# Performance work log

Hardware: AMD Instinct MI355X
Metric: run time of the kernel (lower is better)

Reference implementation:

```python
import jax, jax.numpy as jnp
import numpy as np

H = 16      # num_attention_heads
HKV = 4     # num_key_value_heads
HIDDEN = 1024
HEAD_DIM = HIDDEN // H  # 64
ROPE_BASE = 10000.0


def _rope(x):
    # Rotate-half RoPE applied over the FULL projected last dim, matching the
    # module which applies self._rope before splitting into heads.
    B, S, D = x.shape
    half = D // 2
    inv_freq = 1.0 / (ROPE_BASE ** (jnp.arange(half, dtype=jnp.float32) / half))
    ang = jnp.arange(S, dtype=jnp.float32)[:, None] * inv_freq[None, :]  # [S, half]
    cos, sin = jnp.cos(ang), jnp.sin(ang)
    x1, x2 = x[..., :half], x[..., half:]
    return jnp.concatenate([x1 * cos - x2 * sin, x2 * cos + x1 * sin], axis=-1)


def _rmsnorm(x):
    # F.rms_norm with no weight: x / sqrt(mean(x^2) + eps)
    eps = jnp.finfo(x.dtype).eps
    return x * jax.lax.rsqrt(jnp.mean(x * x, axis=-1, keepdims=True) + eps)


def setup_inputs() -> dict:
    key = jax.random.key(0)
    ks = jax.random.split(key, 10)
    B, S = 2, 2048
    kv_dim = HKV * HEAD_DIM
    sc = 0.02
    return {
        "hidden_state": jax.random.normal(ks[0], (B, S, HIDDEN), dtype=jnp.float32),
        "attention_mask": jnp.zeros((B, S, S), dtype=jnp.float32),
        "Wq": jax.random.normal(ks[1], (HIDDEN, HIDDEN), dtype=jnp.float32) * sc,
        "bq": jnp.zeros((HIDDEN,), dtype=jnp.float32),
        "Wk": jax.random.normal(ks[2], (HIDDEN, kv_dim), dtype=jnp.float32) * sc,
        "bk": jnp.zeros((kv_dim,), dtype=jnp.float32),
        "Wv": jax.random.normal(ks[3], (HIDDEN, kv_dim), dtype=jnp.float32) * sc,
        "bv": jnp.zeros((kv_dim,), dtype=jnp.float32),
        "Wo": jax.random.normal(ks[4], (HIDDEN, HIDDEN), dtype=jnp.float32) * sc,
        "bo": jnp.zeros((HIDDEN,), dtype=jnp.float32),
    }


def reference(hidden_state, attention_mask, Wq, bq, Wk, bk, Wv, bv, Wo, bo):
    B, S, _ = hidden_state.shape
    G = H // HKV  # query heads per kv head
    d = HEAD_DIM

    q = hidden_state @ Wq + bq            # [B,S,H*d]
    k = hidden_state @ Wk + bk            # [B,S,Hkv*d]
    v = hidden_state @ Wv + bv            # [B,S,Hkv*d]

    q = _rope(q)
    k = _rope(k)

    # split heads; repeat_interleave of KV over groups == grouping Q heads as [Hkv, G]
    q = q.reshape(B, S, H, d).transpose(0, 2, 1, 3).reshape(B, HKV, G, S, d)
    k = k.reshape(B, S, HKV, d).transpose(0, 2, 1, 3)   # [B,Hkv,S,d]
    v = v.reshape(B, S, HKV, d).transpose(0, 2, 1, 3)   # [B,Hkv,S,d]

    q = _rmsnorm(q)
    k = _rmsnorm(k)

    scale = d ** 0.5
    scores = jnp.einsum('bkgqd,bksd->bkgqs', q, k) / scale  # [B,Hkv,G,S,S]
    scores = scores + attention_mask[:, None, None, :, :]
    attn = jax.nn.softmax(scores, axis=-1)
    out = jnp.einsum('bkgqs,bksd->bkgqd', attn, v)          # [B,Hkv,G,S,d]

    out = out.reshape(B, H, S, d).transpose(0, 2, 1, 3).reshape(B, S, H * d)
    return out @ Wo + bo
```

## Files before the change

### kernel.cpp

```cpp
#include <hip/hip_runtime.h>
#include <cmath>

#define SEQ 2048
#define BATCH 2
#define HID 1024
#define NH 16
#define NKV 4
#define DH 64
#define KVDIM 256
#define K32C 32

typedef __attribute__((ext_vector_type(8))) short bf16x8;
typedef __attribute__((ext_vector_type(4))) float f32x4;

static __device__ __forceinline__ unsigned short f2bf(float x) {
  union { float f; unsigned u; } v; v.f = x;
  unsigned r = v.u + 0x7fffu + ((v.u >> 16) & 1u);
  return (unsigned short)(r >> 16);
}
static __device__ __forceinline__ float bf2f(unsigned short h) {
  union { unsigned u; float f; } v; v.u = ((unsigned)h) << 16;
  return v.f;
}
static __device__ __forceinline__ void gl_lds16(const unsigned short* g, unsigned short* l) {
  __builtin_amdgcn_global_load_lds(
      (const __attribute__((address_space(1))) unsigned int*)g,
      (__attribute__((address_space(3))) unsigned int*)l, 16, 0, 0);
}

template<bool HILO>
__global__ __launch_bounds__(256) void pack_a_kernel(
    const float* __restrict__ A, unsigned short* __restrict__ hi,
    unsigned short* __restrict__ lo) {
  int gid = blockIdx.x * 256 + threadIdx.x;
  int lane = gid & 63;
  int k32 = (gid >> 6) & 31;
  int m16 = gid >> 11;
  int quad = lane >> 4, l16 = lane & 15;
  const float* src = A + (size_t)(m16 * 16 + l16) * 1024 + k32 * 32 + quad * 8;
  float4 a0 = *(const float4*)src;
  float4 a1 = *(const float4*)(src + 4);
  float v[8] = {a0.x, a0.y, a0.z, a0.w, a1.x, a1.y, a1.z, a1.w};
  unsigned short h[8], l[8];
#pragma unroll
  for (int j = 0; j < 8; ++j) {
    h[j] = f2bf(v[j]);
    if (HILO) l[j] = f2bf(v[j] - bf2f(h[j]));
  }
  *(bf16x8*)(hi + (size_t)gid * 8) = *(bf16x8*)h;
  if (HILO) *(bf16x8*)(lo + (size_t)gid * 8) = *(bf16x8*)l;
}

__global__ __launch_bounds__(256) void pack_a_norm_kernel(
    const float* __restrict__ A, const float* __restrict__ lpart,
    unsigned short* __restrict__ hi, unsigned short* __restrict__ lo) {
  int gid = blockIdx.x * 256 + threadIdx.x;
  int lane = gid & 63;
  int k32 = (gid >> 6) & 31;
  int m16 = gid >> 11;
  int quad = lane >> 4, l16 = lane & 15;
  int m = m16 * 16 + l16;
  int b = m >> 11, s = m & 2047;
  int k0 = k32 * 32 + quad * 8;
  int h = k0 >> 6;
  float inv = 1.0f / lpart[(size_t)(b * NH + h) * SEQ + s];
  const float* src = A + (size_t)m * 1024 + k0;
  float4 a0 = *(const float4*)src;
  float4 a1 = *(const float4*)(src + 4);
  float v[8] = {a0.x, a0.y, a0.z, a0.w, a1.x, a1.y, a1.z, a1.w};
  unsigned short hh[8], ll[8];
#pragma unroll
  for (int j = 0; j < 8; ++j) {
    float x = v[j] * inv;
    hh[j] = f2bf(x);
    ll[j] = f2bf(x - bf2f(hh[j]));
  }
  *(bf16x8*)(hi + (size_t)gid * 8) = *(bf16x8*)hh;
  *(bf16x8*)(lo + (size_t)gid * 8) = *(bf16x8*)ll;
}

template<bool HILO>
__global__ __launch_bounds__(256) void pack_b_kernel(
    const float* __restrict__ W, unsigned short* __restrict__ hi,
    unsigned short* __restrict__ lo, int Nsrc) {
  int gid = blockIdx.x * 256 + threadIdx.x;
  int lane = gid & 63;
  int k32 = (gid >> 6) & 31;
  int n16 = gid >> 11;
  int quad = lane >> 4, l16 = lane & 15;
  int n = n16 * 16 + l16, k = k32 * 32 + quad * 8;
  unsigned short h[8], l[8];
#pragma unroll
  for (int j = 0; j < 8; ++j) {
    float v = W[(size_t)(k + j) * Nsrc + n];
    h[j] = f2bf(v);
    if (HILO) l[j] = f2bf(v - bf2f(h[j]));
  }
  *(bf16x8*)(hi + (size_t)gid * 8) = *(bf16x8*)h;
  if (HILO) *(bf16x8*)(lo + (size_t)gid * 8) = *(bf16x8*)l;
}

__global__ __launch_bounds__(256) void bias_cat_kernel(
    const float* __restrict__ bq, const float* __restrict__ bk,
    const float* __restrict__ bv, float* __restrict__ dst) {
  int n = blockIdx.x * 256 + threadIdx.x;
  if (n < 1536)
    dst[n] = (n < 1024) ? bq[n] : (n < 1280 ? bk[n - 1024] : bv[n - 1280]);
}

template<int CHAINS, bool OUTBF16>
__global__ __launch_bounds__(256) void gemm_pk_kernel(
    const unsigned short* __restrict__ Ah, const unsigned short* __restrict__ Al,
    const unsigned short* __restrict__ Bh, const unsigned short* __restrict__ Bl,
    const float* __restrict__ bias, void* __restrict__ Cout, int N) {
  constexpr int NCH = (CHAINS == 3) ? 2 : 1;
  __shared__ unsigned short Asm[NCH][4 * 512];
  __shared__ unsigned short Bsm[NCH][8 * 512];
  const int tid = threadIdx.x;
  const int wave = tid >> 6, lane = tid & 63;
  const int wr = wave >> 1, wc = wave & 1;
  const int quad = lane >> 4, l16 = lane & 15;
  const size_t abase = ((size_t)(blockIdx.y * 4 + wave) * K32C) * 64 + lane;
  const size_t bbase0 = ((size_t)(blockIdx.x * 8 + wave) * K32C) * 64 + lane;
  const size_t bbase1 = ((size_t)(blockIdx.x * 8 + wave + 4) * K32C) * 64 + lane;
  f32x4 acc[2][4] = {};
  for (int k32 = 0; k32 < K32C; ++k32) {
    __syncthreads();
    gl_lds16(Ah + (abase + (size_t)k32 * 64) * 8, &Asm[0][wave * 512]);
    gl_lds16(Bh + (bbase0 + (size_t)k32 * 64) * 8, &Bsm[0][wave * 512]);
    gl_lds16(Bh + (bbase1 + (size_t)k32 * 64) * 8, &Bsm[0][(wave + 4) * 512]);
    if (CHAINS == 3) {
      gl_lds16(Al + (abase + (size_t)k32 * 64) * 8, &Asm[1][wave * 512]);
      gl_lds16(Bl + (bbase0 + (size_t)k32 * 64) * 8, &Bsm[1][wave * 512]);
      gl_lds16(Bl + (bbase1 + (size_t)k32 * 64) * 8, &Bsm[1][(wave + 4) * 512]);
    }
    __syncthreads();
    bf16x8 af[2][NCH], bfr[4][NCH];
#pragma unroll
    for (int mt = 0; mt < 2; ++mt)
#pragma unroll
      for (int ch = 0; ch < NCH; ++ch)
        af[mt][ch] = *(const bf16x8*)&Asm[ch][((wr * 2 + mt) * 64 + lane) * 8];
#pragma unroll
    for (int nt = 0; nt < 4; ++nt)
#pragma unroll
      for (int ch = 0; ch < NCH; ++ch)
        bfr[nt][ch] = *(const bf16x8*)&Bsm[ch][((wc * 4 + nt) * 64 + lane) * 8];
#pragma unroll
    for (int mt = 0; mt < 2; ++mt)
#pragma unroll
      for (int nt = 0; nt < 4; ++nt) {
        acc[mt][nt] = __builtin_amdgcn_mfma_f32_16x16x32_bf16(af[mt][0], bfr[nt][0], acc[mt][nt], 0, 0, 0);
        if (CHAINS == 3) {
          acc[mt][nt] = __builtin_amdgcn_mfma_f32_16x16x32_bf16(af[mt][1], bfr[nt][0], acc[mt][nt], 0, 0, 0);
          acc[mt][nt] = __builtin_amdgcn_mfma_f32_16x16x32_bf16(af[mt][0], bfr[nt][1], acc[mt][nt], 0, 0, 0);
        }
      }
  }
  const int n0 = blockIdx.x * 128 + wc * 64;
  const int m0 = blockIdx.y * 64 + wr * 32;
#pragma unroll
  for (int mt = 0; mt < 2; ++mt)
#pragma unroll
    for (int nt = 0; nt < 4; ++nt)
#pragma unroll
      for (int r = 0; r < 4; ++r) {
        int gm = m0 + mt * 16 + quad * 4 + r;
        int n = n0 + nt * 16 + l16;
        float v = acc[mt][nt][r] + bias[n];
        if (OUTBF16)
          ((unsigned short*)Cout)[(size_t)gm * N + n] = f2bf(v);
        else
          ((float*)Cout)[(size_t)gm * N + n] = v;
      }
}

__global__ __launch_bounds__(1024) void rope_norm_q_kernel(
    const unsigned short* __restrict__ qkv, unsigned short* __restrict__ Qh,
    unsigned short* __restrict__ Ql) {
  const int s = blockIdx.x, b = blockIdx.y;
  const int t = threadIdx.x;
  const unsigned short* row = qkv + ((size_t)b * SEQ + s) * 1536;
  const int j = t & 511;
  float invf = exp2f((float)j * (-13.287712379549449f / 512.0f));
  float ang = (float)s * invf;
  float c = cosf(ang), sn = sinf(ang);
  float x1 = bf2f(row[j]), x2 = bf2f(row[j + 512]);
  float val = (t < 512) ? (x1 * c - x2 * sn) : (x2 * c + x1 * sn);
  float ss = val * val;
#pragma unroll
  for (int off = 1; off < 64; off <<= 1) ss += __shfl_xor(ss, off);
  float rn = rsqrtf(ss * (1.0f / 64.0f) + 1.1920929e-07f);
  float v = val * rn;
  unsigned short hi = f2bf(v);
  unsigned short lo = f2bf(v - bf2f(hi));
  int h = t >> 6, d = t & 63;
  size_t o = (size_t)(b * NH + h) * 131072 +
             ((((size_t)(s >> 4) * 2 + (d >> 5)) * 64) + ((d >> 3) & 3) * 16 + (s & 15)) * 8 + (d & 7);
  Qh[o] = hi;
  Ql[o] = lo;
}

__global__ __launch_bounds__(256) void rope_norm_kv_kernel(
    const unsigned short* __restrict__ qkv, unsigned short* __restrict__ Kpk,
    unsigned short* __restrict__ Vpk) {
  const int s = blockIdx.x, b = blockIdx.y;
  const int t = threadIdx.x;
  const unsigned short* row = qkv + ((size_t)b * SEQ + s) * 1536;
  const int j = t & 127;
  float invf = exp2f((float)j * (-13.287712379549449f / 128.0f));
  float ang = (float)s * invf;
  float c = cosf(ang), sn = sinf(ang);
  float x1 = bf2f(row[1024 + j]), x2 = bf2f(row[1024 + 128 + j]);
  float val = (t < 128) ? (x1 * c - x2 * sn) : (x2 * c + x1 * sn);
  float ss = val * val;
#pragma unroll
  for (int off = 1; off < 64; off <<= 1) ss += __shfl_xor(ss, off);
  float rn = rsqrtf(ss * (1.0f / 64.0f) + 1.1920929e-07f);
  float kv = val * rn;
  int h = t >> 6, d = t & 63;
  size_t ko = (size_t)(b * NKV + h) * 131072 +
              ((((size_t)(s >> 4) * 2 + (d >> 5)) * 64) + ((d >> 3) & 3) * 16 + (s & 15)) * 8 + (d & 7);
  Kpk[ko] = f2bf(kv);
  size_t vo = (size_t)(b * NKV + h) * 131072 +
              ((((size_t)(d >> 4) * 64 + (s >> 5)) * 64) + ((s >> 3) & 3) * 16 + (d & 15)) * 8 + (s & 7);
  Vpk[vo] = row[1280 + t];
}

__global__ __launch_bounds__(256, 4) void attn_mfma2_kernel(
    const unsigned short* __restrict__ Qh, const unsigned short* __restrict__ Ql,
    const unsigned short* __restrict__ Kpk, const unsigned short* __restrict__ Vpk,
    const float* __restrict__ mask, float* __restrict__ attn_po,
    float* __restrict__ l_part) {
  __shared__ unsigned short Kb[4 * 512];
  __shared__ unsigned short Vb[4 * 512];
  __shared__ float Msk[32][36];
  __shared__ unsigned short Ps[4][32 * 72];

  const int b = blockIdx.z;
  const int kvh = blockIdx.y >> 1, jh = blockIdx.y & 1;
  const int q0 = blockIdx.x * 32;
  const int tid = threadIdx.x, wave = tid >> 6, lane = tid & 63;
  const int quad = lane >> 4, l16 = lane & 15;
  const int h = kvh * 4 + wave;

  bf16x8 qh[2][2], ql[2][2];
  {
    const unsigned short* Qb_h = Qh + (size_t)(b * NH + h) * 131072;
    const unsigned short* Qb_l = Ql + (size_t)(b * NH + h) * 131072;
#pragma unroll
    for (int mt = 0; mt < 2; ++mt)
#pragma unroll
      for (int kf = 0; kf < 2; ++kf) {
        size_t o = ((((size_t)(q0 >> 4) + mt) * 2 + kf) * 64 + lane) * 8;
        qh[mt][kf] = *(const bf16x8*)(Qb_h + o);
        ql[mt][kf] = *(const bf16x8*)(Qb_l + o);
      }
  }

  const unsigned short* Kbase = Kpk + (size_t)(b * NKV + kvh) * 131072;
  const unsigned short* Vbase = Vpk + (size_t)(b * NKV + kvh) * 131072;

  bf16x8 ones;
#pragma unroll
  for (int i = 0; i < 8; ++i) ones[i] = (short)0x3F80;

  f32x4 O[2][4] = {};
  f32x4 lAcc[2] = {};

  const int jbase = jh * (SEQ / 2);
  for (int jc = 0; jc < 32; ++jc) {
    const int j0 = jbase + jc * 32;
    __syncthreads();
    {
      gl_lds16(Kbase + ((((size_t)(j0 >> 4) + (wave >> 1)) * 2 + (wave & 1)) * 64 + lane) * 8,
               &Kb[wave * 512]);
      gl_lds16(Vbase + (((size_t)wave * 64 + (j0 >> 5)) * 64 + lane) * 8,
               &Vb[wave * 512]);
      int mr = tid >> 3, c4 = tid & 7;
      float4 m4 = *(const float4*)(mask + ((size_t)b * SEQ + q0 + mr) * SEQ + j0 + c4 * 4);
      Msk[mr][c4 * 4 + 0] = m4.x - 8.0f;
      Msk[mr][c4 * 4 + 1] = m4.y - 8.0f;
      Msk[mr][c4 * 4 + 2] = m4.z - 8.0f;
      Msk[mr][c4 * 4 + 3] = m4.w - 8.0f;
    }
    __syncthreads();

    bf16x8 kbf[2][2], vbf[4];
#pragma unroll
    for (int nt = 0; nt < 2; ++nt)
#pragma unroll
      for (int kf = 0; kf < 2; ++kf)
        kbf[nt][kf] = *(const bf16x8*)&Kb[((nt * 2 + kf) * 64 + lane) * 8];
#pragma unroll
    for (int d16 = 0; d16 < 4; ++d16)
      vbf[d16] = *(const bf16x8*)&Vb[(d16 * 64 + lane) * 8];

#pragma unroll
    for (int mt = 0; mt < 2; ++mt)
#pragma unroll
      for (int nt = 0; nt < 2; ++nt) {
        f32x4 C = {};
        C = __builtin_amdgcn_mfma_f32_16x16x32_bf16(qh[mt][0], kbf[nt][0], C, 0, 0, 0);
        C = __builtin_amdgcn_mfma_f32_16x16x32_bf16(qh[mt][1], kbf[nt][1], C, 0, 0, 0);
        C = __builtin_amdgcn_mfma_f32_16x16x32_bf16(ql[mt][0], kbf[nt][0], C, 0, 0, 0);
        C = __builtin_amdgcn_mfma_f32_16x16x32_bf16(ql[mt][1], kbf[nt][1], C, 0, 0, 0);
#pragma unroll
        for (int r = 0; r < 4; ++r) {
          int row = mt * 16 + quad * 4 + r;
          float p = __expf(fmaf(C[r], 0.125f, Msk[row][nt * 16 + l16]));
          union { float f; unsigned u; } pu; pu.f = p;
          Ps[wave][row * 72 + nt * 16 + l16] = (unsigned short)((pu.u + 0x8000u) >> 16);
        }
      }

    bf16x8 pa[2];
#pragma unroll
    for (int mt = 0; mt < 2; ++mt)
      pa[mt] = *(const bf16x8*)&Ps[wave][(mt * 16 + l16) * 72 + quad * 8];
#pragma unroll
    for (int mt = 0; mt < 2; ++mt) {
      lAcc[mt] = __builtin_amdgcn_mfma_f32_16x16x32_bf16(pa[mt], ones, lAcc[mt], 0, 0, 0);
#pragma unroll
      for (int nt = 0; nt < 4; ++nt)
        O[mt][nt] = __builtin_amdgcn_mfma_f32_16x16x32_bf16(pa[mt], vbf[nt], O[mt][nt], 0, 0, 0);
    }
  }

#pragma unroll
  for (int mt = 0; mt < 2; ++mt)
#pragma unroll
    for (int r = 0; r < 4; ++r) {
      int s = q0 + mt * 16 + quad * 4 + r;
#pragma unroll
      for (int nt = 0; nt < 4; ++nt)
        atomicAdd(attn_po + ((size_t)b * SEQ + s) * HID + h * DH + nt * 16 + l16,
                  O[mt][nt][r]);
      if (l16 == 0)
        atomicAdd(l_part + (size_t)(b * NH + h) * SEQ + s, lAcc[mt][r]);
    }
}

extern "C" void kernel_launch(void* const* d_in, const int* in_sizes, int n_in,
                              void* d_out, int out_size, void* d_ws, size_t ws_size,
                              hipStream_t stream) {
  const float* hs   = (const float*)d_in[0];
  const float* mask = (const float*)d_in[1];
  const float* Wq   = (const float*)d_in[2];
  const float* bq   = (const float*)d_in[3];
  const float* Wk   = (const float*)d_in[4];
  const float* bk   = (const float*)d_in[5];
  const float* Wv   = (const float*)d_in[6];
  const float* bv   = (const float*)d_in[7];
  const float* Wo   = (const float*)d_in[8];
  const float* bo   = (const float*)d_in[9];
  float* out = (float*)d_out;
  char* ws = (char*)d_ws;
  const size_t MiB = 1048576;

  unsigned short* hs_pk   = (unsigned short*)(ws);
  unsigned short* qkvproj = (unsigned short*)(ws + 8 * MiB);
  float*          attn_po = (float*)(ws);
  float*          l_part  = (float*)(ws + 16 * MiB);
  unsigned short* Wqkv_hi = (unsigned short*)(ws + 20 * MiB);
  unsigned short* Wo_hi   = (unsigned short*)(ws + 20 * MiB);
  unsigned short* Wo_lo   = (unsigned short*)(ws + 22 * MiB);
  unsigned short* Qpk_h   = (unsigned short*)(ws + 24 * MiB);
  unsigned short* Qpk_l   = (unsigned short*)(ws + 32 * MiB);
  unsigned short* ao_hi   = (unsigned short*)(ws + 24 * MiB);
  unsigned short* ao_lo   = (unsigned short*)(ws + 32 * MiB);
  unsigned short* Kpk     = (unsigned short*)(ws + 40 * MiB);
  unsigned short* Vpk     = (unsigned short*)(ws + 42 * MiB);
  float*          bias_c  = (float*)(ws + 44 * MiB);

  pack_a_kernel<false><<<2048, 256, 0, stream>>>(hs, hs_pk, nullptr);
  pack_b_kernel<false><<<512, 256, 0, stream>>>(Wq, Wqkv_hi, nullptr, 1024);
  pack_b_kernel<false><<<128, 256, 0, stream>>>(Wk, Wqkv_hi + (size_t)64 * 2048 * 8, nullptr, 256);
  pack_b_kernel<false><<<128, 256, 0, stream>>>(Wv, Wqkv_hi + (size_t)80 * 2048 * 8, nullptr, 256);
  bias_cat_kernel<<<6, 256, 0, stream>>>(bq, bk, bv, bias_c);

  gemm_pk_kernel<1, true><<<dim3(12, 64), 256, 0, stream>>>(
      hs_pk, nullptr, Wqkv_hi, nullptr, bias_c, qkvproj, 1536);

  pack_b_kernel<true><<<512, 256, 0, stream>>>(Wo, Wo_hi, Wo_lo, 1024);

  rope_norm_q_kernel<<<dim3(SEQ, BATCH), dim3(1024), 0, stream>>>(qkvproj, Qpk_h, Qpk_l);
  rope_norm_kv_kernel<<<dim3(SEQ, BATCH), dim3(256), 0, stream>>>(qkvproj, Kpk, Vpk);

  hipMemsetAsync(ws, 0, 16 * MiB + 262144, stream);
  attn_mfma2_kernel<<<dim3(SEQ / 32, NKV * 2, BATCH), 256, 0, stream>>>(
      Qpk_h, Qpk_l, Kpk, Vpk, mask, attn_po, l_part);

  pack_a_norm_kernel<<<2048, 256, 0, stream>>>(attn_po, l_part, ao_hi, ao_lo);
  gemm_pk_kernel<3, false><<<dim3(8, 64), 256, 0, stream>>>(
      ao_hi, ao_lo, Wo_hi, Wo_lo, bo, out, 1024);
}
```

Baseline: 283.4 us.

## Double-buffer LDS tiles in GEMM and attention, load mask into registers

Both the packed GEMM and the attention kernel now keep two LDS buffers. The next K-chunk (or K/V tile) is issued right after the barrier, while MFMA work runs on the current buffer. This removes the second barrier per iteration and is meant to hide global-to-LDS load latency. The attention kernel also drops the shared mask tile: each lane reads its mask values from global memory straight into registers, saving LDS traffic and a barrier at the cost of less coalesced loads and twice the LDS footprint for K/V, which may affect occupancy.

```diff
diff --git a/kernel.cpp b/kernel.cpp
--- a/kernel.cpp
+++ b/kernel.cpp
@@ -114,8 +114,8 @@
     const unsigned short* __restrict__ Bh, const unsigned short* __restrict__ Bl,
     const float* __restrict__ bias, void* __restrict__ Cout, int N) {
   constexpr int NCH = (CHAINS == 3) ? 2 : 1;
-  __shared__ unsigned short Asm[NCH][4 * 512];
-  __shared__ unsigned short Bsm[NCH][8 * 512];
+  __shared__ unsigned short Asm[2][NCH][4 * 512];
+  __shared__ unsigned short Bsm[2][NCH][8 * 512];
   const int tid = threadIdx.x;
   const int wave = tid >> 6, lane = tid & 63;
   const int wr = wave >> 1, wc = wave & 1;
@@ -124,28 +124,35 @@
   const size_t bbase0 = ((size_t)(blockIdx.x * 8 + wave) * K32C) * 64 + lane;
   const size_t bbase1 = ((size_t)(blockIdx.x * 8 + wave + 4) * K32C) * 64 + lane;
   f32x4 acc[2][4] = {};
+
+  auto stage = [&](int buf, int k32) {
+    gl_lds16(Ah + (abase + (size_t)k32 * 64) * 8, &Asm[buf][0][wave * 512]);
+    gl_lds16(Bh + (bbase0 + (size_t)k32 * 64) * 8, &Bsm[buf][0][wave * 512]);
+    gl_lds16(Bh + (bbase1 + (size_t)k32 * 64) * 8, &Bsm[buf][0][(wave + 4) * 512]);
+    if (CHAINS == 3) {
+      gl_lds16(Al + (abase + (size_t)k32 * 64) * 8, &Asm[buf][1][wave * 512]);
+      gl_lds16(Bl + (bbase0 + (size_t)k32 * 64) * 8, &Bsm[buf][1][wave * 512]);
+      gl_lds16(Bl + (bbase1 + (size_t)k32 * 64) * 8, &Bsm[buf][1][(wave + 4) * 512]);
+    }
+  };
+
+  stage(0, 0);
   for (int k32 = 0; k32 < K32C; ++k32) {
+    const int cur = k32 & 1;
     __syncthreads();
-    gl_lds16(Ah + (abase + (size_t)k32 * 64) * 8, &Asm[0][wave * 512]);
-    gl_lds16(Bh + (bbase0 + (size_t)k32 * 64) * 8, &Bsm[0][wave * 512]);
-    gl_lds16(Bh + (bbase1 + (size_t)k32 * 64) * 8, &Bsm[0][(wave + 4) * 512]);
-    if (CHAINS == 3) {
-      gl_lds16(Al + (abase + (size_t)k32 * 64) * 8, &Asm[1][wave * 512]);
-      gl_lds16(Bl + (bbase0 + (size_t)k32 * 64) * 8, &Bsm[1][wave * 512]);
-      gl_lds16(Bl + (bbase1 + (size_t)k32 * 64) * 8, &Bsm[1][(wave + 4) * 512]);
-    }
-    __syncthreads();
+    if (k32 < K32C - 1) stage(cur ^ 1, k32 + 1);
+
     bf16x8 af[2][NCH], bfr[4][NCH];
 #pragma unroll
     for (int mt = 0; mt < 2; ++mt)
 #pragma unroll
       for (int ch = 0; ch < NCH; ++ch)
-        af[mt][ch] = *(const bf16x8*)&Asm[ch][((wr * 2 + mt) * 64 + lane) * 8];
+        af[mt][ch] = *(const bf16x8*)&Asm[cur][ch][((wr * 2 + mt) * 64 + lane) * 8];
 #pragma unroll
     for (int nt = 0; nt < 4; ++nt)
 #pragma unroll
       for (int ch = 0; ch < NCH; ++ch)
-        bfr[nt][ch] = *(const bf16x8*)&Bsm[ch][((wc * 4 + nt) * 64 + lane) * 8];
+        bfr[nt][ch] = *(const bf16x8*)&Bsm[cur][ch][((wc * 4 + nt) * 64 + lane) * 8];
 #pragma unroll
     for (int mt = 0; mt < 2; ++mt)
 #pragma unroll
@@ -227,14 +234,13 @@
   Vpk[vo] = row[1280 + t];
 }
 
-__global__ __launch_bounds__(256, 4) void attn_mfma2_kernel(
+__global__ __launch_bounds__(256, 4) void attn_mfma3_kernel(
     const unsigned short* __restrict__ Qh, const unsigned short* __restrict__ Ql,
     const unsigned short* __restrict__ Kpk, const unsigned short* __restrict__ Vpk,
     const float* __restrict__ mask, float* __restrict__ attn_po,
     float* __restrict__ l_part) {
-  __shared__ unsigned short Kb[4 * 512];
-  __shared__ unsigned short Vb[4 * 512];
-  __shared__ float Msk[32][36];
+  __shared__ unsigned short Kb[2][4 * 512];
+  __shared__ unsigned short Vb[2][4 * 512];
   __shared__ unsigned short Ps[4][32 * 72];
 
   const int b = blockIdx.z;
@@ -260,6 +266,10 @@
 
   const unsigned short* Kbase = Kpk + (size_t)(b * NKV + kvh) * 131072;
   const unsigned short* Vbase = Vpk + (size_t)(b * NKV + kvh) * 131072;
+  const int jbase = jh * (SEQ / 2);
+
+  const float* mbase = mask + ((size_t)b * SEQ + q0) * SEQ + jbase;
+  const int mlane = (quad * 4) * SEQ + l16;
 
   bf16x8 ones;
 #pragma unroll
@@ -268,33 +278,40 @@
   f32x4 O[2][4] = {};
   f32x4 lAcc[2] = {};
 
-  const int jbase = jh * (SEQ / 2);
+  auto stage = [&](int buf, int jc) {
+    const int j0 = jbase + jc * 32;
+    gl_lds16(Kbase + ((((size_t)(j0 >> 4) + (wave >> 1)) * 2 + (wave & 1)) * 64 + lane) * 8,
+             &Kb[buf][wave * 512]);
+    gl_lds16(Vbase + (((size_t)wave * 64 + (j0 >> 5)) * 64 + lane) * 8,
+             &Vb[buf][wave * 512]);
+  };
+
+  stage(0, 0);
   for (int jc = 0; jc < 32; ++jc) {
-    const int j0 = jbase + jc * 32;
+    const int cur = jc & 1;
     __syncthreads();
-    {
-      gl_lds16(Kbase + ((((size_t)(j0 >> 4) + (wave >> 1)) * 2 + (wave & 1)) * 64 + lane) * 8,
-               &Kb[wave * 512]);
-      gl_lds16(Vbase + (((size_t)wave * 64 + (j0 >> 5)) * 64 + lane) * 8,
-               &Vb[wave * 512]);
-      int mr = tid >> 3, c4 = tid & 7;
-      float4 m4 = *(const float4*)(mask + ((size_t)b * SEQ + q0 + mr) * SEQ + j0 + c4 * 4);
-      Msk[mr][c4 * 4 + 0] = m4.x - 8.0f;
-      Msk[mr][c4 * 4 + 1] = m4.y - 8.0f;
-      Msk[mr][c4 * 4 + 2] = m4.z - 8.0f;
-      Msk[mr][c4 * 4 + 3] = m4.w - 8.0f;
-    }
-    __syncthreads();
+
+    float msub[2][2][4];
+#pragma unroll
+    for (int mt = 0; mt < 2; ++mt)
+#pragma unroll
+      for (int nt = 0; nt < 2; ++nt)
+#pragma unroll
+        for (int r = 0; r < 4; ++r)
+          msub[mt][nt][r] =
+              mbase[(size_t)(mt * 16 + r) * SEQ + mlane + jc * 32 + nt * 16] - 8.0f;
+
+    if (jc < 31) stage(cur ^ 1, jc + 1);
 
     bf16x8 kbf[2][2], vbf[4];
 #pragma unroll
     for (int nt = 0; nt < 2; ++nt)
 #pragma unroll
       for (int kf = 0; kf < 2; ++kf)
-        kbf[nt][kf] = *(const bf16x8*)&Kb[((nt * 2 + kf) * 64 + lane) * 8];
+        kbf[nt][kf] = *(const bf16x8*)&Kb[cur][((nt * 2 + kf) * 64 + lane) * 8];
 #pragma unroll
     for (int d16 = 0; d16 < 4; ++d16)
-      vbf[d16] = *(const bf16x8*)&Vb[(d16 * 64 + lane) * 8];
+      vbf[d16] = *(const bf16x8*)&Vb[cur][(d16 * 64 + lane) * 8];
 
 #pragma unroll
     for (int mt = 0; mt < 2; ++mt)
@@ -308,7 +325,7 @@
 #pragma unroll
         for (int r = 0; r < 4; ++r) {
           int row = mt * 16 + quad * 4 + r;
-          float p = __expf(fmaf(C[r], 0.125f, Msk[row][nt * 16 + l16]));
+          float p = __expf(fmaf(C[r], 0.125f, msub[mt][nt][r]));
           union { float f; unsigned u; } pu; pu.f = p;
           Ps[wave][row * 72 + nt * 16 + l16] = (unsigned short)((pu.u + 0x8000u) >> 16);
         }
@@ -388,7 +405,7 @@
   rope_norm_kv_kernel<<<dim3(SEQ, BATCH), dim3(256), 0, stream>>>(qkvproj, Kpk, Vpk);
 
   hipMemsetAsync(ws, 0, 16 * MiB + 262144, stream);
-  attn_mfma2_kernel<<<dim3(SEQ / 32, NKV * 2, BATCH), 256, 0, stream>>>(
+  attn_mfma3_kernel<<<dim3(SEQ / 32, NKV * 2, BATCH), 256, 0, stream>>>(
       Qpk_h, Qpk_l, Kpk, Vpk, mask, attn_po, l_part);
 
   pack_a_norm_kernel<<<2048, 256, 0, stream>>>(attn_po, l_part, ao_hi, ao_lo);
```

New measurement: 309.4 us. 1.09x slower.

## Double-buffer K/V/mask tiles in attention with async global-to-LDS loads

Applied to the files above, without the earlier changes.

The attention kernel now double-buffers K, V and mask tiles in LDS and prefetches the next chunk while computing the current one, which removes one barrier per iteration. The mask is loaded with direct global-to-LDS copies into an XOR-swizzled layout instead of through registers. The -8 offset moves into the exponent argument. The per-wave P staging buffer shrinks to 16 rows and is reused for each m-tile, lowering LDS use. The risk is a race on the single-barrier schedule, since the prefetch into the other buffer is issued right after the barrier.

```diff
diff --git a/kernel.cpp b/kernel.cpp
--- a/kernel.cpp
+++ b/kernel.cpp
@@ -22,7 +22,7 @@
   union { unsigned u; float f; } v; v.u = ((unsigned)h) << 16;
   return v.f;
 }
-static __device__ __forceinline__ void gl_lds16(const unsigned short* g, unsigned short* l) {
+static __device__ __forceinline__ void gl_lds16(const void* g, void* l) {
   __builtin_amdgcn_global_load_lds(
       (const __attribute__((address_space(1))) unsigned int*)g,
       (__attribute__((address_space(3))) unsigned int*)l, 16, 0, 0);
@@ -227,15 +227,15 @@
   Vpk[vo] = row[1280 + t];
 }
 
-__global__ __launch_bounds__(256, 4) void attn_mfma2_kernel(
+__global__ __launch_bounds__(256, 4) void attn_mfma4_kernel(
     const unsigned short* __restrict__ Qh, const unsigned short* __restrict__ Ql,
     const unsigned short* __restrict__ Kpk, const unsigned short* __restrict__ Vpk,
     const float* __restrict__ mask, float* __restrict__ attn_po,
     float* __restrict__ l_part) {
-  __shared__ unsigned short Kb[4 * 512];
-  __shared__ unsigned short Vb[4 * 512];
-  __shared__ float Msk[32][36];
-  __shared__ unsigned short Ps[4][32 * 72];
+  __shared__ __align__(16) unsigned short Kb[2][4 * 512];
+  __shared__ __align__(16) unsigned short Vb[2][4 * 512];
+  __shared__ __align__(16) float Msk[2][32 * 32];
+  __shared__ __align__(16) unsigned short Ps[4][16 * 72];
 
   const int b = blockIdx.z;
   const int kvh = blockIdx.y >> 1, jh = blockIdx.y & 1;
@@ -260,6 +260,12 @@
 
   const unsigned short* Kbase = Kpk + (size_t)(b * NKV + kvh) * 131072;
   const unsigned short* Vbase = Vpk + (size_t)(b * NKV + kvh) * 131072;
+  const int jbase = jh * (SEQ / 2);
+
+  const float* mbase = mask + ((size_t)b * SEQ + q0) * SEQ + jbase;
+  const int srow = wave * 8 + (lane >> 3);
+  const int ssw = ((srow >> 2) & 3) << 2;
+  const float* msrc0 = mbase + (size_t)srow * SEQ + (((lane & 7) * 4) ^ ssw);
 
   bf16x8 ones;
 #pragma unroll
@@ -268,36 +274,34 @@
   f32x4 O[2][4] = {};
   f32x4 lAcc[2] = {};
 
-  const int jbase = jh * (SEQ / 2);
+  auto stage = [&](int buf, int jc) {
+    const int j0 = jbase + jc * 32;
+    gl_lds16(Kbase + ((((size_t)(j0 >> 4) + (wave >> 1)) * 2 + (wave & 1)) * 64 + lane) * 8,
+             &Kb[buf][wave * 512]);
+    gl_lds16(Vbase + (((size_t)wave * 64 + (j0 >> 5)) * 64 + lane) * 8,
+             &Vb[buf][wave * 512]);
+    gl_lds16(msrc0 + jc * 32, &Msk[buf][wave * 256]);
+  };
+
+  stage(0, 0);
   for (int jc = 0; jc < 32; ++jc) {
-    const int j0 = jbase + jc * 32;
+    const int cur = jc & 1;
     __syncthreads();
-    {
-      gl_lds16(Kbase + ((((size_t)(j0 >> 4) + (wave >> 1)) * 2 + (wave & 1)) * 64 + lane) * 8,
-               &Kb[wave * 512]);
-      gl_lds16(Vbase + (((size_t)wave * 64 + (j0 >> 5)) * 64 + lane) * 8,
-               &Vb[wave * 512]);
-      int mr = tid >> 3, c4 = tid & 7;
-      float4 m4 = *(const float4*)(mask + ((size_t)b * SEQ + q0 + mr) * SEQ + j0 + c4 * 4);
-      Msk[mr][c4 * 4 + 0] = m4.x - 8.0f;
-      Msk[mr][c4 * 4 + 1] = m4.y - 8.0f;
-      Msk[mr][c4 * 4 + 2] = m4.z - 8.0f;
-      Msk[mr][c4 * 4 + 3] = m4.w - 8.0f;
-    }
-    __syncthreads();
+    if (jc < 31) stage(cur ^ 1, jc + 1);
 
     bf16x8 kbf[2][2], vbf[4];
 #pragma unroll
     for (int nt = 0; nt < 2; ++nt)
 #pragma unroll
       for (int kf = 0; kf < 2; ++kf)
-        kbf[nt][kf] = *(const bf16x8*)&Kb[((nt * 2 + kf) * 64 + lane) * 8];
+        kbf[nt][kf] = *(const bf16x8*)&Kb[cur][((nt * 2 + kf) * 64 + lane) * 8];
 #pragma unroll
     for (int d16 = 0; d16 < 4; ++d16)
-      vbf[d16] = *(const bf16x8*)&Vb[(d16 * 64 + lane) * 8];
-
-#pragma unroll
-    for (int mt = 0; mt < 2; ++mt)
+      vbf[d16] = *(const bf16x8*)&Vb[cur][(d16 * 64 + lane) * 8];
+
+    bf16x8 pa[2];
+#pragma unroll
+    for (int mt = 0; mt < 2; ++mt) {
 #pragma unroll
       for (int nt = 0; nt < 2; ++nt) {
         f32x4 C = {};
@@ -307,17 +311,15 @@
         C = __builtin_amdgcn_mfma_f32_16x16x32_bf16(ql[mt][1], kbf[nt][1], C, 0, 0, 0);
 #pragma unroll
         for (int r = 0; r < 4; ++r) {
-          int row = mt * 16 + quad * 4 + r;
-          float p = __expf(fmaf(C[r], 0.125f, Msk[row][nt * 16 + l16]));
+          int row16 = quad * 4 + r;
+          float m = Msk[cur][(mt * 16 + row16) * 32 + nt * 16 + (l16 ^ (quad << 2))];
+          float p = __expf(fmaf(C[r], 0.125f, m) - 8.0f);
           union { float f; unsigned u; } pu; pu.f = p;
-          Ps[wave][row * 72 + nt * 16 + l16] = (unsigned short)((pu.u + 0x8000u) >> 16);
+          Ps[wave][row16 * 72 + nt * 16 + l16] = (unsigned short)((pu.u + 0x8000u) >> 16);
         }
       }
-
-    bf16x8 pa[2];
-#pragma unroll
-    for (int mt = 0; mt < 2; ++mt)
-      pa[mt] = *(const bf16x8*)&Ps[wave][(mt * 16 + l16) * 72 + quad * 8];
+      pa[mt] = *(const bf16x8*)&Ps[wave][l16 * 72 + quad * 8];
+    }
 #pragma unroll
     for (int mt = 0; mt < 2; ++mt) {
       lAcc[mt] = __builtin_amdgcn_mfma_f32_16x16x32_bf16(pa[mt], ones, lAcc[mt], 0, 0, 0);
@@ -388,7 +390,7 @@
   rope_norm_kv_kernel<<<dim3(SEQ, BATCH), dim3(256), 0, stream>>>(qkvproj, Kpk, Vpk);
 
   hipMemsetAsync(ws, 0, 16 * MiB + 262144, stream);
-  attn_mfma2_kernel<<<dim3(SEQ / 32, NKV * 2, BATCH), 256, 0, stream>>>(
+  attn_mfma4_kernel<<<dim3(SEQ / 32, NKV * 2, BATCH), 256, 0, stream>>>(
       Qpk_h, Qpk_l, Kpk, Vpk, mask, attn_po, l_part);
 
   pack_a_norm_kernel<<<2048, 256, 0, stream>>>(attn_po, l_part, ao_hi, ao_lo);
```

Result: slower. 289.2 us (+2.0%).
